# Kernel tuning notes

Measured on AMD Instinct MI355X. Metric: run time of the kernel, lower is better.

The kernel has to match this reference:

```python
import jax, jax.numpy as jnp
import numpy as np

# Mamba defaults (mamba_ssm): expand=2, d_state=16, d_conv=4, dt_rank=ceil(d_model/16)
D_MODEL = 256
DEPTH = 2
D_INNER = 2 * D_MODEL          # 512
D_STATE = 16
D_CONV = 4
DT_RANK = (D_MODEL + 15) // 16  # 16
BATCH = 2
SEQLEN = 2048


def setup_inputs() -> dict:
    key = jax.random.key(0)
    ks = jax.random.split(key, 12)
    s = 0.02
    x = jax.random.normal(ks[0], (BATCH, SEQLEN, D_MODEL), jnp.float32)
    ln_w = jnp.ones((DEPTH, D_MODEL), jnp.float32)
    ln_b = jnp.zeros((DEPTH, D_MODEL), jnp.float32)
    in_proj_w = jax.random.normal(ks[1], (DEPTH, 2 * D_INNER, D_MODEL), jnp.float32) * s
    conv_w = jax.random.normal(ks[2], (DEPTH, D_INNER, 1, D_CONV), jnp.float32) * 0.2
    conv_b = jnp.zeros((DEPTH, D_INNER), jnp.float32)
    x_proj_w = jax.random.normal(ks[3], (DEPTH, DT_RANK + 2 * D_STATE, D_INNER), jnp.float32) * s
    dt_proj_w = jax.random.normal(ks[4], (DEPTH, D_INNER, DT_RANK), jnp.float32) * (DT_RANK ** -0.5)
    # dt bias initialized so softplus(bias) ~ U(1e-3, 1e-1), as in mamba_ssm
    dt = jnp.exp(jax.random.uniform(ks[5], (DEPTH, D_INNER)) * (np.log(0.1) - np.log(1e-3)) + np.log(1e-3))
    dt_proj_b = dt + jnp.log(-jnp.expm1(-dt))  # inverse softplus
    A_log = jnp.log(jnp.broadcast_to(jnp.arange(1, D_STATE + 1, dtype=jnp.float32), (DEPTH, D_INNER, D_STATE)))
    D_param = jnp.ones((DEPTH, D_INNER), jnp.float32)
    out_proj_w = jax.random.normal(ks[6], (DEPTH, D_MODEL, D_INNER), jnp.float32) * s
    return {"x": x, "ln_w": ln_w, "ln_b": ln_b, "in_proj_w": in_proj_w,
            "conv_w": conv_w, "conv_b": conv_b, "x_proj_w": x_proj_w,
            "dt_proj_w": dt_proj_w, "dt_proj_b": dt_proj_b, "A_log": A_log,
            "D_param": D_param, "out_proj_w": out_proj_w}


def _layernorm(x, w, b, eps=1e-5):
    mu = jnp.mean(x, axis=-1, keepdims=True)
    var = jnp.var(x, axis=-1, keepdims=True)
    return (x - mu) * jax.lax.rsqrt(var + eps) * w + b


def _mamba_block(x, lw, lb, ipw, cw, cb, xpw, dpw, dpb, alog, dpar, opw):
    # x: [B, L, D]; returns x + Mamba(LN(x))  (residual handled by caller of stack)
    B, L, _ = x.shape
    h = _layernorm(x, lw, lb)
    xz = jnp.einsum('bld,ed->ble', h, ipw)            # [B, L, 2*d_inner]
    xi, z = jnp.split(xz, 2, axis=-1)
    # depthwise causal conv1d
    xc = jnp.transpose(xi, (0, 2, 1))                 # [B, d_inner, L]
    xc = jax.lax.conv_general_dilated(
        xc, cw, window_strides=(1,), padding=[(D_CONV - 1, 0)],
        feature_group_count=D_INNER, dimension_numbers=('NCH', 'OIH', 'NCH'))
    xc = jax.nn.silu(xc + cb[None, :, None])
    xc = jnp.transpose(xc, (0, 2, 1))                 # [B, L, d_inner]
    # input-dependent SSM parameters
    dbl = jnp.einsum('bld,ed->ble', xc, xpw)          # [B, L, dt_rank+2*d_state]
    dt = dbl[..., :DT_RANK]
    Bs = dbl[..., DT_RANK:DT_RANK + D_STATE]          # [B, L, d_state]
    Cs = dbl[..., DT_RANK + D_STATE:]                 # [B, L, d_state]
    delta = jax.nn.softplus(jnp.einsum('blr,dr->bld', dt, dpw) + dpb)  # [B, L, d_inner]
    A = -jnp.exp(alog)                                # [d_inner, d_state]
    dA = jnp.exp(jnp.einsum('bld,dn->bldn', delta, A))
    dBu = jnp.einsum('bld,bln,bld->bldn', delta, Bs, xc)
    # sequential selective scan over time (time-major)
    dA_t = jnp.moveaxis(dA, 1, 0)
    dBu_t = jnp.moveaxis(dBu, 1, 0)
    C_t = jnp.moveaxis(Cs, 1, 0)
    h0 = jnp.zeros((B, D_INNER, D_STATE), x.dtype)
    def step(hprev, inp):
        dA_, dBu_, C_ = inp
        hnew = dA_ * hprev + dBu_                     # [B, d_inner, d_state]
        y = jnp.einsum('bdn,bn->bd', hnew, C_)        # [B, d_inner]
        return hnew, y
    _, ys = jax.lax.scan(step, h0, (dA_t, dBu_t, C_t))
    y = jnp.moveaxis(ys, 0, 1)                        # [B, L, d_inner]
    y = y + xc * dpar
    y = y * jax.nn.silu(z)
    out = jnp.einsum('ble,de->bld', y, opw)           # [B, L, D]
    return x + out


def reference(x, ln_w, ln_b, in_proj_w, conv_w, conv_b, x_proj_w,
              dt_proj_w, dt_proj_b, A_log, D_param, out_proj_w):
    for i in range(DEPTH):
        x = _mamba_block(x, ln_w[i], ln_b[i], in_proj_w[i], conv_w[i], conv_b[i],
                         x_proj_w[i], dt_proj_w[i], dt_proj_b[i], A_log[i],
                         D_param[i], out_proj_w[i])
    return x
```

## Files before the change

kernel.cpp:

```cpp
#include <hip/hip_runtime.h>
#include <hip/hip_bf16.h>
#include <math.h>

#define D_MODEL 256
#define DEPTH 2
#define D_INNER 512
#define D_STATE 16
#define D_CONV 4
#define DT_RANK 16
#define BATCH 2
#define SEQLEN 2048
#define MROWS (BATCH * SEQLEN)

#define LCH 8
#define NCH 512
#define CPB 256

typedef __attribute__((ext_vector_type(8))) short bf16x8;
typedef __attribute__((ext_vector_type(4))) float f32x4;

__device__ __forceinline__ float silu(float v) {
    return v / (1.0f + __expf(-v));
}

__device__ __forceinline__ ushort f2bf(float f) {
    union { float f; unsigned u; } v; v.f = f;
    unsigned r = v.u + 0x7FFFu + ((v.u >> 16) & 1u);
    return (ushort)(r >> 16);
}

__device__ __forceinline__ float bf2f(ushort u) {
    union { unsigned u; float f; } v; v.u = ((unsigned)u) << 16;
    return v.f;
}

__device__ __forceinline__ float softplus_f(float x) {
    return (x > 20.f) ? x : __logf(1.f + __expf(x));
}

#define XS_STR 260
#define HS_STR 264
#define XC_STR 520

__global__ __launch_bounds__(256) void k_cvt(
    const float* __restrict__ ipw, const float* __restrict__ xpw,
    const float* __restrict__ opw, ushort* __restrict__ ipwT,
    ushort* __restrict__ xpwT, ushort* __restrict__ opwT)
{
    size_t tid = (size_t)blockIdx.x * 256 + threadIdx.x;
    {
        int lyr = (int)(tid >> 16), rem = (int)(tid & 65535);
        int n = rem >> 6, k = (rem & 63) * 4;
        float4 v = *(const float4*)(ipw + ((size_t)lyr * 1024 + n) * 256 + k);
        int nt = n >> 4, r = n & 15, kt = k >> 5, c = k & 31;
        ushort4 o = { f2bf(v.x), f2bf(v.y), f2bf(v.z), f2bf(v.w) };
        *(ushort4*)(ipwT + (size_t)lyr * 262144 + (nt * 8 + kt) * 512 + r * 32 + c) = o;
    }
    if (tid < 12288) {
        int lyr = (int)(tid / 6144), rem = (int)(tid % 6144);
        int n = rem >> 7, k = (rem & 127) * 4;
        float4 v = *(const float4*)(xpw + ((size_t)lyr * 48 + n) * 512 + k);
        int nt = n >> 4, r = n & 15, kt = k >> 5, c = k & 31;
        ushort4 o = { f2bf(v.x), f2bf(v.y), f2bf(v.z), f2bf(v.w) };
        *(ushort4*)(xpwT + (size_t)lyr * 24576 + (nt * 16 + kt) * 512 + r * 32 + c) = o;
    }
    if (tid < 65536) {
        int lyr = (int)(tid >> 15), rem = (int)(tid & 32767);
        int n = rem >> 7, k = (rem & 127) * 4;
        float4 v = *(const float4*)(opw + ((size_t)lyr * 256 + n) * 512 + k);
        int nt = n >> 4, r = n & 15, kt = k >> 5, c = k & 31;
        ushort4 o = { f2bf(v.x), f2bf(v.y), f2bf(v.z), f2bf(v.w) };
        *(ushort4*)(opwT + (size_t)lyr * 131072 + (nt * 16 + kt) * 512 + r * 32 + c) = o;
    }
}

__global__ __launch_bounds__(512, 3) void k_front(
    const float* __restrict__ xin, const float* __restrict__ lnwL,
    const float* __restrict__ lnbL, const ushort* __restrict__ ipwT,
    const float* __restrict__ cwL, const float* __restrict__ cbL,
    const ushort* __restrict__ xpwT, const float* __restrict__ dpwL,
    const float* __restrict__ dpbL, const float* __restrict__ alogL,
    ushort* __restrict__ zsB, ushort* __restrict__ xcB,
    float* __restrict__ dbl, float* __restrict__ Ssum,
    float* __restrict__ sdsum)
{
    const int t = threadIdx.x, bid = blockIdx.x;
    const int lane = t & 63, w = t >> 6, l15 = lane & 15, quad = lane >> 4;
    __shared__ float  xs[11 * XS_STR];
    __shared__ ushort hs[16 * HS_STR];
    __shared__ ushort xi_s[11 * 512];
    __shared__ ushort xc_s[16 * XC_STR];
    __shared__ float  dbl_s[8 * 52];
    int m0 = bid * LCH;

    for (int i = t; i < 11 * 64; i += 512) {
        int r = i >> 6, c = (i & 63) * 4;
        int grow = m0 - 3 + r; if (grow < 0) grow = 0;
        float4 v = *(const float4*)(xin + (size_t)grow * D_MODEL + c);
        *(float4*)&xs[r * XS_STR + c] = v;
    }
    __syncthreads();

    if (t < 11 * 16) {
        int r = t >> 4, ci = t & 15;
        float s = 0.f, sq = 0.f;
        #pragma unroll
        for (int k = 0; k < 16; k++) {
            float v = xs[r * XS_STR + ci + 16 * k];
            s += v; sq += v * v;
        }
        #pragma unroll
        for (int off = 1; off < 16; off <<= 1) {
            s  += __shfl_xor(s, off, 16);
            sq += __shfl_xor(sq, off, 16);
        }
        float mu  = s * (1.0f / 256.f);
        float var = sq * (1.0f / 256.f) - mu * mu;
        float rst = rsqrtf(var + 1e-5f);
        #pragma unroll
        for (int k = 0; k < 16; k++) {
            int c = ci + 16 * k;
            float v = (xs[r * XS_STR + c] - mu) * rst * lnwL[c] + lnbL[c];
            hs[r * HS_STR + c] = f2bf(v);
        }
    }
    __syncthreads();

    {
        bf16x8 af[8];
        #pragma unroll
        for (int k8 = 0; k8 < 8; k8++)
            af[k8] = *(const bf16x8*)&hs[l15 * HS_STR + quad * 8 + k8 * 32];
        f32x4 acc[8];
        #pragma unroll
        for (int f = 0; f < 8; f++) acc[f] = (f32x4){0.f, 0.f, 0.f, 0.f};
        const ushort* wb = ipwT + (size_t)w * 64 * 512 + l15 * 32 + quad * 8;
        #pragma unroll
        for (int k8 = 0; k8 < 8; k8++) {
            #pragma unroll
            for (int f = 0; f < 8; f++) {
                bf16x8 bw = *(const bf16x8*)(wb + (f * 8 + k8) * 512);
                acc[f] = __builtin_amdgcn_mfma_f32_16x16x32_bf16(af[k8], bw, acc[f], 0, 0, 0);
            }
        }
        #pragma unroll
        for (int f = 0; f < 8; f++) {
            int n = w * 128 + f * 16 + l15;
            if (n < 512) {
                #pragma unroll
                for (int r2 = 0; r2 < 4; r2++) {
                    int rl = quad * 4 + r2;
                    if (rl < 11) xi_s[rl * 512 + n] = f2bf(acc[f][r2]);
                }
            } else {
                #pragma unroll
                for (int r2 = 0; r2 < 4; r2++) {
                    int rl = quad * 4 + r2;
                    if (rl >= 3 && rl < 11)
                        zsB[(size_t)(m0 + rl - 3) * D_INNER + (n - 512)] =
                            f2bf(silu(acc[f][r2]));
                }
            }
        }
    }
    __syncthreads();

    {
        float4 cw4 = *(const float4*)(cwL + t * 4);
        float cbv = cbL[t];
        #pragma unroll
        for (int rl = 0; rl < LCH; rl++) {
            int l = (m0 + rl) & (SEQLEN - 1);
            float s = cbv;
            if (l >= 3) s = fmaf(cw4.x, bf2f(xi_s[(rl + 0) * 512 + t]), s);
            if (l >= 2) s = fmaf(cw4.y, bf2f(xi_s[(rl + 1) * 512 + t]), s);
            if (l >= 1) s = fmaf(cw4.z, bf2f(xi_s[(rl + 2) * 512 + t]), s);
            s = fmaf(cw4.w, bf2f(xi_s[(rl + 3) * 512 + t]), s);
            ushort xcv = f2bf(silu(s));
            xc_s[rl * XC_STR + t] = xcv;
            xcB[(size_t)(m0 + rl) * D_INNER + t] = xcv;
        }
    }
    __syncthreads();

    if (w < 3) {
        const ushort* wb = xpwT + (size_t)w * 16 * 512 + l15 * 32 + quad * 8;
        bf16x8 bw[16];
        #pragma unroll
        for (int k8 = 0; k8 < 16; k8++)
            bw[k8] = *(const bf16x8*)(wb + k8 * 512);
        f32x4 acc = (f32x4){0.f, 0.f, 0.f, 0.f};
        #pragma unroll
        for (int k8 = 0; k8 < 16; k8++) {
            bf16x8 af = *(const bf16x8*)&xc_s[l15 * XC_STR + quad * 8 + k8 * 32];
            acc = __builtin_amdgcn_mfma_f32_16x16x32_bf16(af, bw[k8], acc, 0, 0, 0);
        }
        int n = w * 16 + l15;
        #pragma unroll
        for (int r2 = 0; r2 < 4; r2++) {
            int rl = quad * 4 + r2;
            if (rl < LCH) {
                dbl_s[rl * 52 + n] = acc[r2];
                dbl[(size_t)(m0 + rl) * 48 + n] = acc[r2];
            }
        }
    }
    __syncthreads();

    {
        float a[16], wdp[16];
        #pragma unroll
        for (int n = 0; n < 16; n++) a[n] = -__expf(alogL[(size_t)t * 16 + n]);
        *(float4*)&wdp[0]  = *(const float4*)(dpwL + (size_t)t * 16 + 0);
        *(float4*)&wdp[4]  = *(const float4*)(dpwL + (size_t)t * 16 + 4);
        *(float4*)&wdp[8]  = *(const float4*)(dpwL + (size_t)t * 16 + 8);
        *(float4*)&wdp[12] = *(const float4*)(dpwL + (size_t)t * 16 + 12);
        float bias = dpbL[t];
        float h[16];
        #pragma unroll
        for (int n = 0; n < 16; n++) h[n] = 0.f;
        float sd = 0.f;
        for (int j = 0; j < LCH; j++) {
            const float* dp = &dbl_s[j * 52];
            float d0 = 0.f, d1 = 0.f;
            #pragma unroll
            for (int r2 = 0; r2 < 8; r2++) {
                d0 = fmaf(dp[r2], wdp[r2], d0);
                d1 = fmaf(dp[8 + r2], wdp[8 + r2], d1);
            }
            float dl = softplus_f(bias + d0 + d1);
            float xv = bf2f(xc_s[j * XC_STR + t]);
            float u = dl * xv;
            sd += dl;
            #pragma unroll
            for (int n = 0; n < 16; n++)
                h[n] = fmaf(__expf(dl * a[n]), h[n], dp[16 + n] * u);
        }
        size_t sbase = (size_t)bid * 16 * D_INNER + t;
        #pragma unroll
        for (int n = 0; n < 16; n++) Ssum[sbase + (size_t)n * D_INNER] = h[n];
        sdsum[(size_t)bid * D_INNER + t] = sd;
    }
}

__global__ __launch_bounds__(512, 4) void k_comb(
    const float* __restrict__ alogL, const float* __restrict__ sdsum,
    float* __restrict__ Ssum)
{
    const int t = threadIdx.x, bid = blockIdx.x;
    __shared__ float S_l[32][17], sd_l[32][17];
    int ch32 = t & 31, seg = t >> 5;
    int chain = bid * 32 + ch32;
    int d = chain & 511;
    int n = (chain >> 9) & 15;
    int b = chain >> 13;
    float a = -__expf(alogL[(size_t)d * 16 + n]);
    int c0 = b * CPB + seg * 16;

    float s_r[16], sd_r[16];
    float S = 0.f, sdt = 0.f;
    #pragma unroll
    for (int j = 0; j < 16; j++) {
        size_t c = (size_t)(c0 + j);
        float s  = Ssum[(c * 16 + n) * D_INNER + d];
        float sd = sdsum[c * D_INNER + d];
        s_r[j] = s; sd_r[j] = sd;
        S = fmaf(__expf(a * sd), S, s);
        sdt += sd;
    }
    S_l[ch32][seg] = S;
    sd_l[ch32][seg] = sdt;
    __syncthreads();

    if (t < 32) {
        float hi = 0.f;
        #pragma unroll
        for (int g = 0; g < 16; g++) {
            float Sv = S_l[t][g], sdv = sd_l[t][g];
            S_l[t][g] = hi;
            hi = fmaf(__expf(a * sdv), hi, Sv);
        }
    }
    __syncthreads();

    float hi = S_l[ch32][seg];
    #pragma unroll
    for (int j = 0; j < 16; j++) {
        size_t c = (size_t)(c0 + j);
        Ssum[(c * 16 + n) * D_INNER + d] = hi;
        hi = fmaf(__expf(a * sd_r[j]), hi, s_r[j]);
    }
}

__global__ __launch_bounds__(512, 3) void k_back(
    const float* __restrict__ dbl, const ushort* __restrict__ xcB,
    const ushort* __restrict__ zsB, const float* __restrict__ Ssum,
    const float* __restrict__ dpwL, const float* __restrict__ dpbL,
    const float* __restrict__ alogL, const float* __restrict__ dparL,
    const ushort* __restrict__ opwT, const float* __restrict__ xin,
    float* __restrict__ xout)
{
    const int t = threadIdx.x, bid = blockIdx.x;
    const int lane = t & 63, w = t >> 6, l15 = lane & 15, quad = lane >> 4;
    __shared__ ushort yy_s[16 * XC_STR];
    __shared__ float  dbl_l[8 * 48];
    int m0 = bid * LCH;

    if (t < 8 * 48) dbl_l[t] = dbl[(size_t)m0 * 48 + t];
    __syncthreads();

    {
        float a[16], wdp[16];
        #pragma unroll
        for (int n = 0; n < 16; n++) a[n] = -__expf(alogL[(size_t)t * 16 + n]);
        *(float4*)&wdp[0]  = *(const float4*)(dpwL + (size_t)t * 16 + 0);
        *(float4*)&wdp[4]  = *(const float4*)(dpwL + (size_t)t * 16 + 4);
        *(float4*)&wdp[8]  = *(const float4*)(dpwL + (size_t)t * 16 + 8);
        *(float4*)&wdp[12] = *(const float4*)(dpwL + (size_t)t * 16 + 12);
        float bias = dpbL[t];
        float Dd = dparL[t];
        float h[16];
        size_t sbase = (size_t)bid * 16 * D_INNER + t;
        #pragma unroll
        for (int n = 0; n < 16; n++) h[n] = Ssum[sbase + (size_t)n * D_INNER];
        for (int j = 0; j < LCH; j++) {
            int row = m0 + j;
            const float* dp = &dbl_l[j * 48];
            float d0 = 0.f, d1 = 0.f;
            #pragma unroll
            for (int r2 = 0; r2 < 8; r2++) {
                d0 = fmaf(dp[r2], wdp[r2], d0);
                d1 = fmaf(dp[8 + r2], wdp[8 + r2], d1);
            }
            float dl = softplus_f(bias + d0 + d1);
            float xv = bf2f(xcB[(size_t)row * D_INNER + t]);
            float gate = bf2f(zsB[(size_t)row * D_INNER + t]);
            float u = dl * xv;
            float y0 = 0.f, y1 = 0.f, y2 = 0.f, y3 = 0.f;
            #pragma unroll
            for (int q = 0; q < 4; q++) {
                h[4 * q + 0] = fmaf(__expf(dl * a[4 * q + 0]), h[4 * q + 0], dp[16 + 4 * q + 0] * u);
                h[4 * q + 1] = fmaf(__expf(dl * a[4 * q + 1]), h[4 * q + 1], dp[16 + 4 * q + 1] * u);
                h[4 * q + 2] = fmaf(__expf(dl * a[4 * q + 2]), h[4 * q + 2], dp[16 + 4 * q + 2] * u);
                h[4 * q + 3] = fmaf(__expf(dl * a[4 * q + 3]), h[4 * q + 3], dp[16 + 4 * q + 3] * u);
                y0 = fmaf(h[4 * q + 0], dp[32 + 4 * q + 0], y0);
                y1 = fmaf(h[4 * q + 1], dp[32 + 4 * q + 1], y1);
                y2 = fmaf(h[4 * q + 2], dp[32 + 4 * q + 2], y2);
                y3 = fmaf(h[4 * q + 3], dp[32 + 4 * q + 3], y3);
            }
            float y = (y0 + y1) + (y2 + y3) + xv * Dd;
            yy_s[j * XC_STR + t] = f2bf(y * gate);
        }
    }
    __syncthreads();

    {
        bf16x8 af[16];
        #pragma unroll
        for (int k8 = 0; k8 < 16; k8++)
            af[k8] = *(const bf16x8*)&yy_s[l15 * XC_STR + quad * 8 + k8 * 32];
        f32x4 acc0 = (f32x4){0.f, 0.f, 0.f, 0.f};
        f32x4 acc1 = (f32x4){0.f, 0.f, 0.f, 0.f};
        const ushort* wb = opwT + (size_t)w * 2 * 16 * 512 + l15 * 32 + quad * 8;
        #pragma unroll
        for (int k8 = 0; k8 < 16; k8++) {
            bf16x8 b0 = *(const bf16x8*)(wb + k8 * 512);
            bf16x8 b1 = *(const bf16x8*)(wb + (16 + k8) * 512);
            acc0 = __builtin_amdgcn_mfma_f32_16x16x32_bf16(af[k8], b0, acc0, 0, 0, 0);
            acc1 = __builtin_amdgcn_mfma_f32_16x16x32_bf16(af[k8], b1, acc1, 0, 0, 0);
        }
        #pragma unroll
        for (int f = 0; f < 2; f++) {
            int n = w * 32 + f * 16 + l15;
            const f32x4& acc = (f == 0) ? acc0 : acc1;
            #pragma unroll
            for (int r2 = 0; r2 < 4; r2++) {
                int rl = quad * 4 + r2;
                if (rl < LCH) {
                    int row = m0 + rl;
                    xout[(size_t)row * D_MODEL + n] =
                        acc[r2] + xin[(size_t)row * D_MODEL + n];
                }
            }
        }
    }
}

extern "C" void kernel_launch(void* const* d_in, const int* in_sizes, int n_in,
                              void* d_out, int out_size, void* d_ws, size_t ws_size,
                              hipStream_t stream)
{
    const float* x    = (const float*)d_in[0];
    const float* lnw  = (const float*)d_in[1];
    const float* lnb  = (const float*)d_in[2];
    const float* ipw  = (const float*)d_in[3];
    const float* cw   = (const float*)d_in[4];
    const float* cb   = (const float*)d_in[5];
    const float* xpw  = (const float*)d_in[6];
    const float* dpw  = (const float*)d_in[7];
    const float* dpb  = (const float*)d_in[8];
    const float* alog = (const float*)d_in[9];
    const float* dpar = (const float*)d_in[10];
    const float* opw  = (const float*)d_in[11];
    float* out = (float*)d_out;

    char* p = (char*)d_ws;
    auto alloc = [&](size_t bytes) { char* r = p; p += (bytes + 255) & ~(size_t)255; return r; };
    ushort* zsB   = (ushort*)alloc((size_t)MROWS * D_INNER * 2);
    ushort* xcB   = (ushort*)alloc((size_t)MROWS * D_INNER * 2);
    float*  dbl   = (float*)alloc((size_t)MROWS * 48 * 4);
    float*  Ssum  = (float*)alloc((size_t)NCH * 16 * D_INNER * 4);
    float*  sdsum = (float*)alloc((size_t)NCH * D_INNER * 4);
    ushort* ipwT  = (ushort*)alloc((size_t)DEPTH * 262144 * 2);
    ushort* xpwT  = (ushort*)alloc((size_t)DEPTH * 24576 * 2);
    ushort* opwT  = (ushort*)alloc((size_t)DEPTH * 131072 * 2);

    k_cvt<<<512, 256, 0, stream>>>(ipw, xpw, opw, ipwT, xpwT, opwT);

    for (int lyr = 0; lyr < DEPTH; lyr++) {
        const float* xin = (lyr == 0) ? x : out;
        float* xout = out;
        const float* alogL = alog + (size_t)lyr * D_INNER * D_STATE;
        const float* dpwL  = dpw + (size_t)lyr * D_INNER * DT_RANK;
        const float* dpbL  = dpb + lyr * D_INNER;

        k_front<<<NCH, 512, 0, stream>>>(
            xin, lnw + lyr * D_MODEL, lnb + lyr * D_MODEL,
            ipwT + (size_t)lyr * 262144,
            cw + (size_t)lyr * D_INNER * D_CONV, cb + lyr * D_INNER,
            xpwT + (size_t)lyr * 24576, dpwL, dpbL, alogL,
            zsB, xcB, dbl, Ssum, sdsum);

        k_comb<<<512, 512, 0, stream>>>(alogL, sdsum, Ssum);

        k_back<<<NCH, 512, 0, stream>>>(
            dbl, xcB, zsB, Ssum, dpwL, dpbL, alogL,
            dpar + lyr * D_INNER,
            opwT + (size_t)lyr * 131072, xin, xout);
    }
}
```

Measured before the change: 207.6 us.

## Fuse front, combine and back kernels into one persistent kernel with grid barriers

Merges the three per-layer kernels into a single kernel that uses an atomic-counter grid barrier between the chunk-scan, cross-chunk combine and output phases. Intermediates (conv output, gated z, x_proj results) now stay in shared memory instead of round-tripping through global buffers, and shared memory is reused across phases through one aliased buffer. This removes two launches per layer and the global write and read of those intermediates. In exchange it relies on all 512 blocks being co-resident for the spin barrier to make progress, and it adds barrier spin overhead.

```diff
diff --git a/kernel.cpp b/kernel.cpp
--- a/kernel.cpp
+++ b/kernel.cpp
@@ -38,6 +38,17 @@
     return (x > 20.f) ? x : __logf(1.f + __expf(x));
 }
 
+__device__ __forceinline__ void gridbar(unsigned* bar, unsigned target) {
+    __syncthreads();
+    if (threadIdx.x == 0) {
+        __threadfence();
+        __hip_atomic_fetch_add(bar, 1u, __ATOMIC_RELEASE, __HIP_MEMORY_SCOPE_AGENT);
+        while (__hip_atomic_load(bar, __ATOMIC_ACQUIRE, __HIP_MEMORY_SCOPE_AGENT) < target)
+            __builtin_amdgcn_s_sleep(2);
+    }
+    __syncthreads();
+}
+
 #define XS_STR 260
 #define HS_STR 264
 #define XC_STR 520
@@ -45,9 +56,11 @@
 __global__ __launch_bounds__(256) void k_cvt(
     const float* __restrict__ ipw, const float* __restrict__ xpw,
     const float* __restrict__ opw, ushort* __restrict__ ipwT,
-    ushort* __restrict__ xpwT, ushort* __restrict__ opwT)
+    ushort* __restrict__ xpwT, ushort* __restrict__ opwT,
+    unsigned* __restrict__ bar)
 {
     size_t tid = (size_t)blockIdx.x * 256 + threadIdx.x;
+    if (tid == 0) *bar = 0u;
     {
         int lyr = (int)(tid >> 16), rem = (int)(tid & 65535);
         int n = rem >> 6, k = (rem & 63) * 4;
@@ -74,23 +87,31 @@
     }
 }
 
-__global__ __launch_bounds__(512, 3) void k_front(
+__global__ __launch_bounds__(512, 4) void k_fused(
     const float* __restrict__ xin, const float* __restrict__ lnwL,
     const float* __restrict__ lnbL, const ushort* __restrict__ ipwT,
     const float* __restrict__ cwL, const float* __restrict__ cbL,
     const ushort* __restrict__ xpwT, const float* __restrict__ dpwL,
     const float* __restrict__ dpbL, const float* __restrict__ alogL,
-    ushort* __restrict__ zsB, ushort* __restrict__ xcB,
-    float* __restrict__ dbl, float* __restrict__ Ssum,
-    float* __restrict__ sdsum)
+    const float* __restrict__ dparL, const ushort* __restrict__ opwT,
+    float* __restrict__ Ssum, float* __restrict__ sdsum,
+    unsigned* __restrict__ bar, unsigned epoch0,
+    float* __restrict__ xout)
 {
     const int t = threadIdx.x, bid = blockIdx.x;
     const int lane = t & 63, w = t >> 6, l15 = lane & 15, quad = lane >> 4;
-    __shared__ float  xs[11 * XS_STR];
-    __shared__ ushort hs[16 * HS_STR];
-    __shared__ ushort xi_s[11 * 512];
-    __shared__ ushort xc_s[16 * XC_STR];
-    __shared__ float  dbl_s[8 * 52];
+
+    __shared__ __align__(16) char smem[57664];
+    float*  xs    = (float*)(smem);
+    ushort* hs    = (ushort*)(smem + 11456);
+    ushort* yy_s  = (ushort*)(smem);
+    ushort* xi_s  = (ushort*)(smem + 19904);
+    float*  S_l   = (float*)(smem + 19904);
+    float*  sd_l  = (float*)(smem + 22080);
+    ushort* xc_s  = (ushort*)(smem + 31168);
+    ushort* z_s   = (ushort*)(smem + 47808);
+    float*  dbl_s = (float*)(smem + 56000);
+
     int m0 = bid * LCH;
 
     for (int i = t; i < 11 * 64; i += 512) {
@@ -157,8 +178,7 @@
                 for (int r2 = 0; r2 < 4; r2++) {
                     int rl = quad * 4 + r2;
                     if (rl >= 3 && rl < 11)
-                        zsB[(size_t)(m0 + rl - 3) * D_INNER + (n - 512)] =
-                            f2bf(silu(acc[f][r2]));
+                        z_s[(rl - 3) * 512 + (n - 512)] = f2bf(silu(acc[f][r2]));
                 }
             }
         }
@@ -176,9 +196,7 @@
             if (l >= 2) s = fmaf(cw4.y, bf2f(xi_s[(rl + 1) * 512 + t]), s);
             if (l >= 1) s = fmaf(cw4.z, bf2f(xi_s[(rl + 2) * 512 + t]), s);
             s = fmaf(cw4.w, bf2f(xi_s[(rl + 3) * 512 + t]), s);
-            ushort xcv = f2bf(silu(s));
-            xc_s[rl * XC_STR + t] = xcv;
-            xcB[(size_t)(m0 + rl) * D_INNER + t] = xcv;
+            xc_s[rl * XC_STR + t] = f2bf(silu(s));
         }
     }
     __syncthreads();
@@ -199,23 +217,21 @@
         #pragma unroll
         for (int r2 = 0; r2 < 4; r2++) {
             int rl = quad * 4 + r2;
-            if (rl < LCH) {
-                dbl_s[rl * 52 + n] = acc[r2];
-                dbl[(size_t)(m0 + rl) * 48 + n] = acc[r2];
-            }
-        }
-    }
-    __syncthreads();
-
-    {
-        float a[16], wdp[16];
+            if (rl < LCH) dbl_s[rl * 52 + n] = acc[r2];
+        }
+    }
+    __syncthreads();
+
+    float a[16], wdp[16], bias, Dd;
+    {
         #pragma unroll
         for (int n = 0; n < 16; n++) a[n] = -__expf(alogL[(size_t)t * 16 + n]);
         *(float4*)&wdp[0]  = *(const float4*)(dpwL + (size_t)t * 16 + 0);
         *(float4*)&wdp[4]  = *(const float4*)(dpwL + (size_t)t * 16 + 4);
         *(float4*)&wdp[8]  = *(const float4*)(dpwL + (size_t)t * 16 + 8);
         *(float4*)&wdp[12] = *(const float4*)(dpwL + (size_t)t * 16 + 12);
-        float bias = dpbL[t];
+        bias = dpbL[t];
+        Dd = dparL[t];
         float h[16];
         #pragma unroll
         for (int n = 0; n < 16; n++) h[n] = 0.f;
@@ -241,91 +257,62 @@
         for (int n = 0; n < 16; n++) Ssum[sbase + (size_t)n * D_INNER] = h[n];
         sdsum[(size_t)bid * D_INNER + t] = sd;
     }
-}
-
-__global__ __launch_bounds__(512, 4) void k_comb(
-    const float* __restrict__ alogL, const float* __restrict__ sdsum,
-    float* __restrict__ Ssum)
-{
-    const int t = threadIdx.x, bid = blockIdx.x;
-    __shared__ float S_l[32][17], sd_l[32][17];
-    int ch32 = t & 31, seg = t >> 5;
-    int chain = bid * 32 + ch32;
-    int d = chain & 511;
-    int n = (chain >> 9) & 15;
-    int b = chain >> 13;
-    float a = -__expf(alogL[(size_t)d * 16 + n]);
-    int c0 = b * CPB + seg * 16;
-
-    float s_r[16], sd_r[16];
-    float S = 0.f, sdt = 0.f;
-    #pragma unroll
-    for (int j = 0; j < 16; j++) {
-        size_t c = (size_t)(c0 + j);
-        float s  = Ssum[(c * 16 + n) * D_INNER + d];
-        float sd = sdsum[c * D_INNER + d];
-        s_r[j] = s; sd_r[j] = sd;
-        S = fmaf(__expf(a * sd), S, s);
-        sdt += sd;
-    }
-    S_l[ch32][seg] = S;
-    sd_l[ch32][seg] = sdt;
-    __syncthreads();
-
-    if (t < 32) {
-        float hi = 0.f;
-        #pragma unroll
-        for (int g = 0; g < 16; g++) {
-            float Sv = S_l[t][g], sdv = sd_l[t][g];
-            S_l[t][g] = hi;
-            hi = fmaf(__expf(a * sdv), hi, Sv);
-        }
-    }
-    __syncthreads();
-
-    float hi = S_l[ch32][seg];
-    #pragma unroll
-    for (int j = 0; j < 16; j++) {
-        size_t c = (size_t)(c0 + j);
-        Ssum[(c * 16 + n) * D_INNER + d] = hi;
-        hi = fmaf(__expf(a * sd_r[j]), hi, s_r[j]);
-    }
-}
-
-__global__ __launch_bounds__(512, 3) void k_back(
-    const float* __restrict__ dbl, const ushort* __restrict__ xcB,
-    const ushort* __restrict__ zsB, const float* __restrict__ Ssum,
-    const float* __restrict__ dpwL, const float* __restrict__ dpbL,
-    const float* __restrict__ alogL, const float* __restrict__ dparL,
-    const ushort* __restrict__ opwT, const float* __restrict__ xin,
-    float* __restrict__ xout)
-{
-    const int t = threadIdx.x, bid = blockIdx.x;
-    const int lane = t & 63, w = t >> 6, l15 = lane & 15, quad = lane >> 4;
-    __shared__ ushort yy_s[16 * XC_STR];
-    __shared__ float  dbl_l[8 * 48];
-    int m0 = bid * LCH;
-
-    if (t < 8 * 48) dbl_l[t] = dbl[(size_t)m0 * 48 + t];
-    __syncthreads();
-
-    {
-        float a[16], wdp[16];
-        #pragma unroll
-        for (int n = 0; n < 16; n++) a[n] = -__expf(alogL[(size_t)t * 16 + n]);
-        *(float4*)&wdp[0]  = *(const float4*)(dpwL + (size_t)t * 16 + 0);
-        *(float4*)&wdp[4]  = *(const float4*)(dpwL + (size_t)t * 16 + 4);
-        *(float4*)&wdp[8]  = *(const float4*)(dpwL + (size_t)t * 16 + 8);
-        *(float4*)&wdp[12] = *(const float4*)(dpwL + (size_t)t * 16 + 12);
-        float bias = dpbL[t];
-        float Dd = dparL[t];
+
+    gridbar(bar, (epoch0 + 1) * NCH);
+
+    {
+        int ch32 = t & 31, seg = t >> 5;
+        int chain = bid * 32 + ch32;
+        int d = chain & 511;
+        int n = (chain >> 9) & 15;
+        int b = chain >> 13;
+        float ac = -__expf(alogL[(size_t)d * 16 + n]);
+        int c0 = b * CPB + seg * 16;
+
+        float s_r[16], sd_r[16];
+        float S = 0.f, sdt = 0.f;
+        #pragma unroll
+        for (int j = 0; j < 16; j++) {
+            size_t c = (size_t)(c0 + j);
+            float s  = Ssum[(c * 16 + n) * D_INNER + d];
+            float sv = sdsum[c * D_INNER + d];
+            s_r[j] = s; sd_r[j] = sv;
+            S = fmaf(__expf(ac * sv), S, s);
+            sdt += sv;
+        }
+        S_l[ch32 * 17 + seg] = S;
+        sd_l[ch32 * 17 + seg] = sdt;
+        __syncthreads();
+
+        if (t < 32) {
+            float hi = 0.f;
+            #pragma unroll
+            for (int g = 0; g < 16; g++) {
+                float Sv = S_l[t * 17 + g], sdv = sd_l[t * 17 + g];
+                S_l[t * 17 + g] = hi;
+                hi = fmaf(__expf(ac * sdv), hi, Sv);
+            }
+        }
+        __syncthreads();
+
+        float hi = S_l[ch32 * 17 + seg];
+        #pragma unroll
+        for (int j = 0; j < 16; j++) {
+            size_t c = (size_t)(c0 + j);
+            Ssum[(c * 16 + n) * D_INNER + d] = hi;
+            hi = fmaf(__expf(ac * sd_r[j]), hi, s_r[j]);
+        }
+    }
+
+    gridbar(bar, (epoch0 + 2) * NCH);
+
+    {
         float h[16];
         size_t sbase = (size_t)bid * 16 * D_INNER + t;
         #pragma unroll
         for (int n = 0; n < 16; n++) h[n] = Ssum[sbase + (size_t)n * D_INNER];
         for (int j = 0; j < LCH; j++) {
-            int row = m0 + j;
-            const float* dp = &dbl_l[j * 48];
+            const float* dp = &dbl_s[j * 48 == j * 48 ? j * 52 : 0];
             float d0 = 0.f, d1 = 0.f;
             #pragma unroll
             for (int r2 = 0; r2 < 8; r2++) {
@@ -333,8 +320,8 @@
                 d1 = fmaf(dp[8 + r2], wdp[8 + r2], d1);
             }
             float dl = softplus_f(bias + d0 + d1);
-            float xv = bf2f(xcB[(size_t)row * D_INNER + t]);
-            float gate = bf2f(zsB[(size_t)row * D_INNER + t]);
+            float xv = bf2f(xc_s[j * XC_STR + t]);
+            float gate = bf2f(z_s[j * 512 + t]);
             float u = dl * xv;
             float y0 = 0.f, y1 = 0.f, y2 = 0.f, y3 = 0.f;
             #pragma unroll
@@ -406,36 +393,27 @@
 
     char* p = (char*)d_ws;
     auto alloc = [&](size_t bytes) { char* r = p; p += (bytes + 255) & ~(size_t)255; return r; };
-    ushort* zsB   = (ushort*)alloc((size_t)MROWS * D_INNER * 2);
-    ushort* xcB   = (ushort*)alloc((size_t)MROWS * D_INNER * 2);
-    float*  dbl   = (float*)alloc((size_t)MROWS * 48 * 4);
     float*  Ssum  = (float*)alloc((size_t)NCH * 16 * D_INNER * 4);
     float*  sdsum = (float*)alloc((size_t)NCH * D_INNER * 4);
     ushort* ipwT  = (ushort*)alloc((size_t)DEPTH * 262144 * 2);
     ushort* xpwT  = (ushort*)alloc((size_t)DEPTH * 24576 * 2);
     ushort* opwT  = (ushort*)alloc((size_t)DEPTH * 131072 * 2);
-
-    k_cvt<<<512, 256, 0, stream>>>(ipw, xpw, opw, ipwT, xpwT, opwT);
+    unsigned* bar = (unsigned*)alloc(256);
+
+    k_cvt<<<512, 256, 0, stream>>>(ipw, xpw, opw, ipwT, xpwT, opwT, bar);
 
     for (int lyr = 0; lyr < DEPTH; lyr++) {
         const float* xin = (lyr == 0) ? x : out;
         float* xout = out;
-        const float* alogL = alog + (size_t)lyr * D_INNER * D_STATE;
-        const float* dpwL  = dpw + (size_t)lyr * D_INNER * DT_RANK;
-        const float* dpbL  = dpb + lyr * D_INNER;
-
-        k_front<<<NCH, 512, 0, stream>>>(
+
+        k_fused<<<NCH, 512, 0, stream>>>(
             xin, lnw + lyr * D_MODEL, lnb + lyr * D_MODEL,
             ipwT + (size_t)lyr * 262144,
             cw + (size_t)lyr * D_INNER * D_CONV, cb + lyr * D_INNER,
-            xpwT + (size_t)lyr * 24576, dpwL, dpbL, alogL,
-            zsB, xcB, dbl, Ssum, sdsum);
-
-        k_comb<<<512, 512, 0, stream>>>(alogL, sdsum, Ssum);
-
-        k_back<<<NCH, 512, 0, stream>>>(
-            dbl, xcB, zsB, Ssum, dpwL, dpbL, alogL,
-            dpar + lyr * D_INNER,
-            opwT + (size_t)lyr * 131072, xin, xout);
-    }
-}
+            xpwT + (size_t)lyr * 24576,
+            dpw + (size_t)lyr * D_INNER * DT_RANK, dpb + lyr * D_INNER,
+            alog + (size_t)lyr * D_INNER * D_STATE, dpar + lyr * D_INNER,
+            opwT + (size_t)lyr * 131072,
+            Ssum, sdsum, bar, (unsigned)(lyr * 2), xout);
+    }
+}
```

After: 475.8 us. 129% more time.
